# Kernel optimization log

Hardware: AMD Instinct MI355X
Metric: run time of the kernel (lower is better)

Reference implementation:

```python
import jax, jax.numpy as jnp
import numpy as np

KERNEL_SIZE = 5
SIGMA_INTENSITY = 0.1
SIGMA_SPATIAL = 1.0
EPS = 1e-8


def make_spatial_kernel():
    coords = jnp.arange(KERNEL_SIZE, dtype=jnp.float32) - KERNEL_SIZE // 2
    x, y = jnp.meshgrid(coords, coords, indexing='ij')
    return jnp.exp(-(x ** 2 + y ** 2) / (2.0 * SIGMA_SPATIAL ** 2))


def setup_inputs() -> dict:
    key = jax.random.key(0)
    images = jax.random.uniform(key, (16, 3, 512, 512), dtype=jnp.float32)
    spatial_kernel = make_spatial_kernel()
    return {"images": images, "spatial_kernel": spatial_kernel}


def reference(images, spatial_kernel):
    B, C, H, W = images.shape
    K = KERNEL_SIZE
    p = K // 2
    # reflect pad (torch 'reflect' == jnp 'reflect', edge not repeated)
    padded = jnp.pad(images, ((0, 0), (0, 0), (p, p), (p, p)), mode='reflect')
    # extract K*K shifted views -> (B, C, K*K, H, W); fixed small loop over offsets
    patches = jnp.stack(
        [padded[:, :, i:i + H, j:j + W] for i in range(K) for j in range(K)],
        axis=2,
    )
    center_idx = K * K // 2
    center = patches[:, :, center_idx:center_idx + 1, :, :]
    diff = patches - center
    intensity_w = jnp.exp(-(diff ** 2) / (2.0 * SIGMA_INTENSITY ** 2))
    spatial_flat = spatial_kernel.reshape(1, 1, K * K, 1, 1)
    w = spatial_flat * intensity_w
    w = w / (jnp.sum(w, axis=2, keepdims=True) + EPS)
    filtered = jnp.sum(patches * w, axis=2)  # (B, C, H, W)
    return filtered
```

## Files before the change

### kernel.cpp

```cpp
#include <hip/hip_runtime.h>
#include <stdint.h>

#define IMG 512
#define KS2 24598.990f

typedef float v2f  __attribute__((ext_vector_type(2)));
typedef int   v2i  __attribute__((ext_vector_type(2)));
typedef float v2fu __attribute__((ext_vector_type(2), aligned(4)));

__device__ __forceinline__ int reflect_idx(int g) {
    int a = abs(g);
    return min(a, 2 * IMG - 2 - a);
}

__global__ __launch_bounds__(256, 4) void bilateral_main(
    const float* __restrict__ img, float* __restrict__ out)
{
    const int plane = blockIdx.z;
    const int pi = blockIdx.x * 64 + threadIdx.x;
    const int xp = 2 + 2 * pi;
    if (xp > 508) return;
    const int yb = (blockIdx.y * 4 + threadIdx.y) * 4;

    const float* __restrict__ src = img + (size_t)plane * (IMG * IMG);

    v2f P[8][5];
    #pragma unroll
    for (int r = 0; r < 8; ++r) {
        const float* rp = src + reflect_idx(yb - 2 + r) * IMG + (xp - 2);
        #pragma unroll
        for (int k = 0; k < 5; ++k)
            P[r][k] = *reinterpret_cast<const v2fu*>(rp + k);
    }

    const uint32_t ksb = __builtin_bit_cast(uint32_t, KS2);
    const uint64_t kspair = (uint64_t)ksb * 0x100000001ULL;

    float* const dst = out + (size_t)plane * (IMG * IMG) + (size_t)yb * IMG + xp;

    #pragma unroll
    for (int p = 0; p < 4; ++p) {
        v2f qc = P[p + 2][2];
        v2f qcs;
        asm("v_pk_mul_f32 %0, %1, %2" : "=v"(qcs) : "s"(kspair), "v"(qc));
        v2f wsum = {1.0f, 1.0f};
        v2f acc  = qc;

        #pragma unroll
        for (int dy = 0; dy < 5; ++dy) {
            #pragma unroll
            for (int dx = 0; dx < 5; ++dx) {
                if (dy == 2 && dx == 2) continue;
                const int r2 = (dx - 2) * (dx - 2) + (dy - 2) * (dy - 2);
                const float    Kf    = (float)(1065353216.0 - 6051101.63118 * (double)r2);
                const uint32_t kb    = __builtin_bit_cast(uint32_t, Kf);
                const uint64_t kpair = (uint64_t)kb * 0x100000001ULL;

                v2f qt = P[p + dy][dx];
                v2f ds, t;
                asm("v_pk_fma_f32 %0, %1, %2, %3 neg_lo:[0,0,1] neg_hi:[0,0,1]"
                    : "=v"(ds) : "s"(kspair), "v"(qt), "v"(qcs));
                asm("v_pk_fma_f32 %0, %1, %1, %2 neg_lo:[1,0,0] neg_hi:[1,0,0]"
                    : "=v"(t) : "v"(ds), "s"(kpair));
                v2i iv = __builtin_convertvector(t, v2i);
                v2f e  = __builtin_bit_cast(v2f, iv);
                asm("v_pk_add_f32 %0, %1, %0" : "+v"(wsum) : "v"(e));
                asm("v_pk_fma_f32 %0, %1, %2, %0" : "+v"(acc) : "v"(e), "v"(qt));
            }
        }
        v2f res;
        res.x = acc.x * __builtin_amdgcn_rcpf(wsum.x);
        res.y = acc.y * __builtin_amdgcn_rcpf(wsum.y);
        *reinterpret_cast<v2f*>(dst + p * IMG) = res;
    }
}

__global__ __launch_bounds__(256) void bilateral_edge(
    const float* __restrict__ img, float* __restrict__ out)
{
    const int idx = blockIdx.x * 256 + threadIdx.x;
    const int plane = idx >> 11;
    const int rem   = idx & 2047;
    const int y  = rem >> 2;
    const int xi = rem & 3;
    const int x  = (xi < 2) ? xi : (IMG - 4 + xi);

    const float* __restrict__ src = img + (size_t)plane * (IMG * IMG);
    const float qc = src[y * IMG + x];
    float wsum = 1.0f, acc = qc;

    #pragma unroll
    for (int dy = 0; dy < 5; ++dy) {
        const int yy = reflect_idx(y + dy - 2) * IMG;
        #pragma unroll
        for (int dx = 0; dx < 5; ++dx) {
            if (dy == 2 && dx == 2) continue;
            const int r2 = (dx - 2) * (dx - 2) + (dy - 2) * (dy - 2);
            const float Kf = (float)(1065353216.0 - 6051101.63118 * (double)r2);
            const float qt = src[yy + reflect_idx(x + dx - 2)];
            const float d  = (qt - qc) * KS2;
            const float t  = __builtin_fmaf(-d, d, Kf);
            const float e  = __builtin_bit_cast(float, (int)t);
            wsum += e;
            acc = __builtin_fmaf(e, qt, acc);
        }
    }
    out[(size_t)plane * (IMG * IMG) + y * IMG + x] = acc * __builtin_amdgcn_rcpf(wsum);
}

extern "C" void kernel_launch(void* const* d_in, const int* in_sizes, int n_in,
                              void* d_out, int out_size, void* d_ws, size_t ws_size,
                              hipStream_t stream) {
    const float* img = (const float*)d_in[0];
    float* out = (float*)d_out;
    const int planes = in_sizes[0] / (IMG * IMG);

    dim3 gmain(4, 32, planes);
    dim3 bmain(64, 4, 1);
    bilateral_main<<<gmain, bmain, 0, stream>>>(img, out);

    const int edge_threads = planes * IMG * 4;
    bilateral_edge<<<edge_threads / 256, 256, 0, stream>>>(img, out);
}
```

Baseline: 132.3 us.

## Stage pre-scaled input tiles in LDS instead of per-thread register windows

The main kernel now has each block load a 12x68 reflect-padded tile into shared memory. The tile is pre-multiplied by the intensity scale, which removes one multiply per tap and is undone by a final multiply at the output. Each thread computes one row of two pixels from LDS instead of loading an 8x5 register window to produce four rows. This trades redundant global loads and register pressure for LDS traffic and a block barrier. Each thread also does less work, so more blocks are launched.

```diff
diff --git a/kernel.cpp b/kernel.cpp
--- a/kernel.cpp
+++ b/kernel.cpp
@@ -2,7 +2,14 @@
 #include <stdint.h>
 
 #define IMG 512
-#define KS2 24598.990f
+#define KS2     24598.990f
+#define INV_KS2 4.0652061e-05f
+
+#define TW  64
+#define TH  8
+#define LWD 68
+#define LW  69
+#define LH  12
 
 typedef float v2f  __attribute__((ext_vector_type(2)));
 typedef int   v2i  __attribute__((ext_vector_type(2)));
@@ -13,66 +20,70 @@
     return min(a, 2 * IMG - 2 - a);
 }
 
-__global__ __launch_bounds__(256, 4) void bilateral_main(
+__global__ __launch_bounds__(256) void bilateral_main(
     const float* __restrict__ img, float* __restrict__ out)
 {
+    __shared__ float q[LH][LW];
+
     const int plane = blockIdx.z;
-    const int pi = blockIdx.x * 64 + threadIdx.x;
-    const int xp = 2 + 2 * pi;
-    if (xp > 508) return;
-    const int yb = (blockIdx.y * 4 + threadIdx.y) * 4;
-
+    const int x0 = 2 + blockIdx.x * TW;
+    const int y0 = blockIdx.y * TH;
     const float* __restrict__ src = img + (size_t)plane * (IMG * IMG);
 
-    v2f P[8][5];
-    #pragma unroll
-    for (int r = 0; r < 8; ++r) {
-        const float* rp = src + reflect_idx(yb - 2 + r) * IMG + (xp - 2);
-        #pragma unroll
-        for (int k = 0; k < 5; ++k)
-            P[r][k] = *reinterpret_cast<const v2fu*>(rp + k);
-    }
-
-    const uint32_t ksb = __builtin_bit_cast(uint32_t, KS2);
-    const uint64_t kspair = (uint64_t)ksb * 0x100000001ULL;
-
-    float* const dst = out + (size_t)plane * (IMG * IMG) + (size_t)yb * IMG + xp;
+    const int tx = threadIdx.x, ty = threadIdx.y;
+    const int tid = tx + ty * 32;
 
     #pragma unroll
     for (int p = 0; p < 4; ++p) {
-        v2f qc = P[p + 2][2];
-        v2f qcs;
-        asm("v_pk_mul_f32 %0, %1, %2" : "=v"(qcs) : "s"(kspair), "v"(qc));
-        v2f wsum = {1.0f, 1.0f};
-        v2f acc  = qc;
+        int idx = tid + p * 256;
+        if (idx < LH * LWD) {
+            int r = idx / LWD;
+            int c = idx - r * LWD;
+            q[r][c] = src[reflect_idx(y0 - 2 + r) * IMG
+                          + reflect_idx(x0 - 2 + c)] * KS2;
+        }
+    }
+    __syncthreads();
 
+    const int xp = x0 + 2 * tx;
+    if (xp > 508) return;
+
+    const float* cp = &q[ty + 2][2 * tx];
+    v2f qc = *reinterpret_cast<const v2fu*>(cp + 2);
+
+    v2f wsum = {1.0f, 1.0f};
+    v2f acc  = qc;
+
+    #pragma unroll
+    for (int dy = 0; dy < 5; ++dy) {
+        const float* rp = &q[ty + dy][2 * tx];
         #pragma unroll
-        for (int dy = 0; dy < 5; ++dy) {
-            #pragma unroll
-            for (int dx = 0; dx < 5; ++dx) {
-                if (dy == 2 && dx == 2) continue;
-                const int r2 = (dx - 2) * (dx - 2) + (dy - 2) * (dy - 2);
-                const float    Kf    = (float)(1065353216.0 - 6051101.63118 * (double)r2);
-                const uint32_t kb    = __builtin_bit_cast(uint32_t, Kf);
-                const uint64_t kpair = (uint64_t)kb * 0x100000001ULL;
+        for (int dx = 0; dx < 5; ++dx) {
+            if (dy == 2 && dx == 2) continue;
+            const int r2 = (dx - 2) * (dx - 2) + (dy - 2) * (dy - 2);
+            const float    Kf    = (float)(1065353216.0 - 6051101.63118 * (double)r2);
+            const uint32_t kb    = __builtin_bit_cast(uint32_t, Kf);
+            const uint64_t kpair = (uint64_t)kb * 0x100000001ULL;
 
-                v2f qt = P[p + dy][dx];
-                v2f ds, t;
-                asm("v_pk_fma_f32 %0, %1, %2, %3 neg_lo:[0,0,1] neg_hi:[0,0,1]"
-                    : "=v"(ds) : "s"(kspair), "v"(qt), "v"(qcs));
-                asm("v_pk_fma_f32 %0, %1, %1, %2 neg_lo:[1,0,0] neg_hi:[1,0,0]"
-                    : "=v"(t) : "v"(ds), "s"(kpair));
-                v2i iv = __builtin_convertvector(t, v2i);
-                v2f e  = __builtin_bit_cast(v2f, iv);
-                asm("v_pk_add_f32 %0, %1, %0" : "+v"(wsum) : "v"(e));
-                asm("v_pk_fma_f32 %0, %1, %2, %0" : "+v"(acc) : "v"(e), "v"(qt));
-            }
+            v2f qt = *reinterpret_cast<const v2fu*>(rp + dx);
+            v2f d, t;
+            asm("v_pk_add_f32 %0, %1, %2 neg_lo:[0,1] neg_hi:[0,1]"
+                : "=v"(d) : "v"(qt), "v"(qc));
+            asm("v_pk_fma_f32 %0, %1, %1, %2 neg_lo:[1,0,0] neg_hi:[1,0,0]"
+                : "=v"(t) : "v"(d), "s"(kpair));
+            v2i iv = __builtin_convertvector(t, v2i);
+            v2f e  = __builtin_bit_cast(v2f, iv);
+            asm("v_pk_add_f32 %0, %1, %0" : "+v"(wsum) : "v"(e));
+            asm("v_pk_fma_f32 %0, %1, %2, %0" : "+v"(acc) : "v"(e), "v"(qt));
         }
-        v2f res;
-        res.x = acc.x * __builtin_amdgcn_rcpf(wsum.x);
-        res.y = acc.y * __builtin_amdgcn_rcpf(wsum.y);
-        *reinterpret_cast<v2f*>(dst + p * IMG) = res;
     }
+
+    v2f res;
+    res.x = acc.x * __builtin_amdgcn_rcpf(wsum.x) * INV_KS2;
+    res.y = acc.y * __builtin_amdgcn_rcpf(wsum.y) * INV_KS2;
+
+    float* dst = out + (size_t)plane * (IMG * IMG) + (size_t)(y0 + ty) * IMG + xp;
+    *reinterpret_cast<v2f*>(dst) = res;
 }
 
 __global__ __launch_bounds__(256) void bilateral_edge(
@@ -115,8 +126,8 @@
     float* out = (float*)d_out;
     const int planes = in_sizes[0] / (IMG * IMG);
 
-    dim3 gmain(4, 32, planes);
-    dim3 bmain(64, 4, 1);
+    dim3 gmain((508 + TW - 1) / TW, IMG / TH, planes);
+    dim3 bmain(32, 8, 1);
     bilateral_main<<<gmain, bmain, 0, stream>>>(img, out);
 
     const int edge_threads = planes * IMG * 4;
```

After: 137.7 us. 4.1% more time.
